# Kernel optimization log

Hardware: AMD Instinct MI355X
Metric: run time of the kernel (lower is better)

Reference implementation:

```python
import jax, jax.numpy as jnp
import numpy as np

N = 100000
E = 1600000
IN_DIM = 128
OUT_DIM = 128
NEG_SLOPE = 0.01  # F.leaky_relu default


def setup_inputs() -> dict:
    key = jax.random.key(0)
    k1, k2, k3, k4, k5, k6 = jax.random.split(key, 6)
    feat = jax.random.normal(k1, (N, IN_DIM), dtype=jnp.float32)
    biclique_mask = jax.random.uniform(k2, (IN_DIM,), dtype=jnp.float32)
    W = jax.random.normal(k3, (OUT_DIM, IN_DIM), dtype=jnp.float32) * 0.05
    attn = jax.random.normal(k4, (OUT_DIM,), dtype=jnp.float32) * 0.1
    src = jax.random.randint(k5, (E,), 0, N, dtype=jnp.int32)
    dst = jax.random.randint(k6, (E,), 0, N, dtype=jnp.int32)
    return {"feat": feat, "biclique_mask": biclique_mask, "W": W,
            "attn": attn, "src": src, "dst": dst}


def reference(feat, biclique_mask, W, attn, src, dst):
    # h = Linear(feat * mask), no bias
    h = (feat * biclique_mask[None, :]) @ W.T            # [N, out_dim]
    # edge score depends only on src node -> compute per-node then gather
    s = jax.nn.leaky_relu(h @ attn, negative_slope=NEG_SLOPE)  # [N]
    score = s[src]                                        # [E]
    # edge softmax grouped by destination node
    seg_max = jax.ops.segment_max(score, dst, num_segments=N)  # [N]
    seg_max = jnp.where(jnp.isfinite(seg_max), seg_max, 0.0)   # empty segs
    ex = jnp.exp(score - seg_max[dst])                     # [E]
    denom = jax.ops.segment_sum(ex, dst, num_segments=N)   # [N]
    a = ex / denom[dst]                                    # [E]
    # weighted aggregation: sum_{e: dst(e)=v} h[src(e)] * a[e]
    m = h[src] * a[:, None]                                # [E, out_dim]
    h_new = jax.ops.segment_sum(m, dst, num_segments=N)    # [N, out_dim]
    return jax.nn.relu(h_new)
```

## Files before the change

kernel.cpp:

```cpp
#include <hip/hip_runtime.h>
#include <math.h>

#define NN 100000
#define EE 1600000
#define DIM 128

#define BK 256
#define NBK2 392
#define NCH 256
#define EPB 6250
#define SCN (NBK2 * NCH)
#define NSB 98

#define GEMM_BLKS 782
#define FBLK 512

#define LDS_ROW 272
#define LDS_B_OFF 34816
#define LDS_TOT 69632

#define SRC_MASK 0x1FFFFu

typedef _Float16 half8 __attribute__((ext_vector_type(8)));
typedef _Float16 half4v __attribute__((ext_vector_type(4)));
typedef signed char char8 __attribute__((ext_vector_type(8)));
typedef float f32x4 __attribute__((ext_vector_type(4)));

__global__ __launch_bounds__(256) void k_wt(const float* __restrict__ W,
                                            const float* __restrict__ mask,
                                            _Float16* __restrict__ Bt) {
    int o = blockIdx.x * 256 + threadIdx.x;
    if (o < DIM * DIM) Bt[o] = (_Float16)(W[o] * mask[o & 127]);
}

__global__ __launch_bounds__(512, 4) void k_front(const float* __restrict__ feat,
                                                  const _Float16* __restrict__ Bt,
                                                  const float* __restrict__ attn,
                                                  signed char* __restrict__ hq,
                                                  float* __restrict__ scf,
                                                  _Float16* __restrict__ sv16,
                                                  const int* __restrict__ dst,
                                                  int* __restrict__ gHist) {
    __shared__ char smem[LDS_TOT];
    const int bx = blockIdx.x;
    const int t  = threadIdx.x;

    if (bx >= GEMM_BLKS) {
        int* hist = (int*)smem;
        const int b = bx - GEMM_BLKS;
        for (int i = t; i < NBK2; i += FBLK) hist[i] = 0;
        __syncthreads();
        const int e0 = b * EPB;
        int e1 = e0 + EPB; if (e1 > EE) e1 = EE;
        for (int e = e0 + t; e < e1; e += FBLK)
            atomicAdd(&hist[dst[e] >> 8], 1);
        __syncthreads();
        for (int i = t; i < NBK2; i += FBLK)
            gHist[i * NCH + b] = hist[i];
        return;
    }

    const int rowBase = bx * 128;

#pragma unroll
    for (int i = 0; i < 8; ++i) {
        int idx  = i * FBLK + t;
        int r    = idx >> 5;
        int c4   = idx & 31;
        int rowg = rowBase + r;
        float4 f = (rowg < NN)
                       ? ((const float4*)(feat + (size_t)rowg * DIM))[c4]
                       : make_float4(0.f, 0.f, 0.f, 0.f);
        half4v h;
        h[0] = (_Float16)f.x; h[1] = (_Float16)f.y;
        h[2] = (_Float16)f.z; h[3] = (_Float16)f.w;
        *(half4v*)(smem + r * LDS_ROW + c4 * 8) = h;
    }
#pragma unroll
    for (int i = 0; i < 4; ++i) {
        int idx = i * FBLK + t;
        int r   = idx >> 4;
        int c8  = idx & 15;
        int4 v = ((const int4*)(Bt + (size_t)r * DIM))[c8];
        *(int4*)(smem + LDS_B_OFF + r * LDS_ROW + c8 * 16) = v;
    }
    __syncthreads();

    const int lane = t & 63;
    const int wv   = t >> 6;
    const int l15  = lane & 15;
    const int quad = lane >> 4;
    const int row0 = rowBase + wv * 16;

    f32x4 acc[8];
#pragma unroll
    for (int nt = 0; nt < 8; ++nt) acc[nt] = (f32x4){0.f, 0.f, 0.f, 0.f};

    const char* Abase = smem + (wv * 16 + l15) * LDS_ROW + quad * 16;
    const char* Bbase = smem + LDS_B_OFF + l15 * LDS_ROW + quad * 16;

#pragma unroll
    for (int kc = 0; kc < 4; ++kc) {
        half8 a = *(const half8*)(Abase + kc * 64);
#pragma unroll
        for (int nt = 0; nt < 8; ++nt) {
            half8 b = *(const half8*)(Bbase + nt * 16 * LDS_ROW + kc * 64);
            acc[nt] = __builtin_amdgcn_mfma_f32_16x16x32_f16(a, b, acc[nt], 0, 0, 0);
        }
    }

    float avv[8];
#pragma unroll
    for (int nt = 0; nt < 8; ++nt) avv[nt] = attn[nt * 16 + l15];

    char* qslice = smem + wv * (16 * LDS_ROW);
#pragma unroll
    for (int r = 0; r < 4; ++r) {
        int row = row0 + quad * 4 + r;
        float p = 0.f, m = 0.f;
#pragma unroll
        for (int nt = 0; nt < 8; ++nt) {
            p += acc[nt][r] * avv[nt];
            m = fmaxf(m, fabsf(acc[nt][r]));
        }
        p += __shfl_xor(p, 1, 64);
        p += __shfl_xor(p, 2, 64);
        p += __shfl_xor(p, 4, 64);
        p += __shfl_xor(p, 8, 64);
        m = fmaxf(m, __shfl_xor(m, 1, 64));
        m = fmaxf(m, __shfl_xor(m, 2, 64));
        m = fmaxf(m, __shfl_xor(m, 4, 64));
        m = fmaxf(m, __shfl_xor(m, 8, 64));
        if (l15 == 0 && row < NN) {
            float lr = (p > 0.f) ? p : 0.01f * p;
            sv16[row] = (_Float16)__expf(lr);
            scf[row]  = m * (1.f / 127.f);
        }
        const float inv_s = (m > 0.f) ? (127.f / m) : 0.f;
#pragma unroll
        for (int nt = 0; nt < 8; ++nt) {
            float qv = rintf(acc[nt][r] * inv_s);
            qv = fminf(fmaxf(qv, -127.f), 127.f);
            qslice[(quad * 4 + r) * 128 + nt * 16 + l15] = (signed char)(int)qv;
        }
    }
    {
        const int rowg = row0 + (lane >> 2);
        if (rowg < NN) {
            int4 v0 = *(const int4*)(qslice + lane * 32);
            int4 v1 = *(const int4*)(qslice + lane * 32 + 16);
            int4* dp = (int4*)(hq + (size_t)rowg * DIM + (lane & 3) * 32);
            dp[0] = v0;
            dp[1] = v1;
        }
    }
}

__global__ __launch_bounds__(256) void k_scan_a(const int* __restrict__ deg,
                                                int* __restrict__ excl,
                                                int* __restrict__ bsum) {
    __shared__ int wsum[4];
    __shared__ int woff[4];
    const int t = threadIdx.x, b = blockIdx.x;
    const int base = b * 1024 + t * 4;
    int v0 = deg[base + 0];
    int v1 = deg[base + 1];
    int v2 = deg[base + 2];
    int v3 = deg[base + 3];
    int tsum = v0 + v1 + v2 + v3;

    const int lane = t & 63, w = t >> 6;
    int incl = tsum;
#pragma unroll
    for (int d = 1; d < 64; d <<= 1) {
        int n = __shfl_up(incl, d, 64);
        if (lane >= d) incl += n;
    }
    if (lane == 63) wsum[w] = incl;
    __syncthreads();
    if (t == 0) {
        int run = 0;
#pragma unroll
        for (int i = 0; i < 4; ++i) { woff[i] = run; run += wsum[i]; }
        bsum[b] = run;
    }
    __syncthreads();
    int texcl = incl - tsum + woff[w];
    excl[base + 0] = texcl;
    excl[base + 1] = texcl + v0;
    excl[base + 2] = texcl + v0 + v1;
    excl[base + 3] = texcl + v0 + v1 + v2;
}

#define INLINE_BOFF_SCAN(bsum, sboff, swtop, t)                          \
    {                                                                    \
        const int lane_ = (t) & 63;                                      \
        int v_ = 0, incl_ = 0;                                           \
        if ((t) < 128) {                                                 \
            v_ = ((t) < NSB) ? (bsum)[(t)] : 0;                          \
            incl_ = v_;                                                  \
            _Pragma("unroll")                                            \
            for (int d_ = 1; d_ < 64; d_ <<= 1) {                        \
                int n_ = __shfl_up(incl_, d_, 64);                       \
                if (lane_ >= d_) incl_ += n_;                            \
            }                                                            \
            if ((t) == 63) (swtop) = incl_;                              \
        }                                                                \
        __syncthreads();                                                 \
        if ((t) < NSB) {                                                 \
            int add_ = ((t) >= 64) ? (swtop) : 0;                        \
            (sboff)[(t)] = incl_ - v_ + add_;                            \
        }                                                                \
        __syncthreads();                                                 \
    }

__global__ __launch_bounds__(1024) void k_bscatter(const int* __restrict__ src,
                                                   const int* __restrict__ dst,
                                                   const int* __restrict__ gOff,
                                                   const int* __restrict__ bsum,
                                                   unsigned* __restrict__ binned) {
    __shared__ int cur[NBK2];
    __shared__ int sboff[NSB];
    __shared__ int swtop;
    const int t = threadIdx.x, b = blockIdx.x;

    INLINE_BOFF_SCAN(bsum, sboff, swtop, t)

    for (int i = t; i < NBK2; i += 1024) {
        int idx = i * NCH + b;
        cur[i] = gOff[idx] + sboff[idx >> 10];
    }
    __syncthreads();
    const int e0 = b * EPB;
    int e1 = e0 + EPB; if (e1 > EE) e1 = EE;
    for (int e = e0 + t; e < e1; e += 1024) {
        int d  = dst[e];
        int si = src[e];
        int bk   = d >> 8;
        int dloc = d & (BK - 1);
        int pos = atomicAdd(&cur[bk], 1);
        binned[pos] = (unsigned)si | ((unsigned)dloc << 17);
    }
}

__global__ __launch_bounds__(1024) void k_group(const int* __restrict__ gOff,
                                                const int* __restrict__ bsum,
                                                const unsigned* __restrict__ binned,
                                                const _Float16* __restrict__ sv16,
                                                const float* __restrict__ scf,
                                                unsigned* __restrict__ pack,
                                                int* __restrict__ offs,
                                                float* __restrict__ lsum) {
    __shared__ int ldeg[BK];
    __shared__ float lsumSh[BK];
    __shared__ int wpart[4];
    __shared__ int sboff[NSB];
    __shared__ int swtop;
    const int bk = blockIdx.x;
    const int t  = threadIdx.x;

    INLINE_BOFF_SCAN(bsum, sboff, swtop, t)

    const int i0 = bk * NCH;
    const int base = gOff[i0] + sboff[i0 >> 10];
    int endp;
    if (bk == NBK2 - 1) endp = EE;
    else {
        int i1 = (bk + 1) * NCH;
        endp = gOff[i1] + sboff[i1 >> 10];
    }

    if (t < BK) { ldeg[t] = 0; lsumSh[t] = 0.f; }
    __syncthreads();
    for (int j = base + t; j < endp; j += 1024)
        atomicAdd(&ldeg[(binned[j] >> 17) & (BK - 1)], 1);
    __syncthreads();

    int v = 0, incl = 0;
    const int lane = t & 63;
    if (t < BK) {
        v = ldeg[t];
        incl = v;
#pragma unroll
        for (int d = 1; d < 64; d <<= 1) {
            int n = __shfl_up(incl, d, 64);
            if (lane >= d) incl += n;
        }
        if (lane == 63) wpart[t >> 6] = incl;
    }
    __syncthreads();
    if (t == 0) {
        int run = 0;
#pragma unroll
        for (int i = 0; i < 4; ++i) { int tmp = wpart[i]; wpart[i] = run; run += tmp; }
    }
    __syncthreads();
    if (t < BK) {
        int excl = incl - v + wpart[t >> 6];
        int c = base + excl;
        int n = bk * BK + t;
        if (n < NN) offs[n] = c;
        ldeg[t] = c;
    }
    if (bk == NBK2 - 1 && t == 0) offs[NN] = EE;
    __syncthreads();

    for (int j = base + t; j < endp; j += 1024) {
        unsigned e = binned[j];
        int dloc = (e >> 17) & (BK - 1);
        int si   = e & SRC_MASK;
        float w  = (float)sv16[si];
        float sc = scf[si];
        unsigned short wb =
            __builtin_bit_cast(unsigned short, (_Float16)(w * sc));
        atomicAdd(&lsumSh[dloc], w);
        int pos = atomicAdd(&ldeg[dloc], 1);
        pack[pos] = (unsigned)si | ((unsigned)wb << 17);
    }
    __syncthreads();
    if (t < BK) {
        int n = bk * BK + t;
        if (n < NN) lsum[n] = lsumSh[t];
    }
}

__global__ __launch_bounds__(256) void k_agg(const signed char* __restrict__ hq,
                                             const int* __restrict__ offs,
                                             const unsigned* __restrict__ pack,
                                             const float* __restrict__ lsum,
                                             float* __restrict__ out) {
    const int lane = threadIdx.x & 63;
    const int g    = lane >> 4;
    const int li   = lane & 15;
    const int wid  = __builtin_amdgcn_readfirstlane(blockIdx.x * 4 + (threadIdx.x >> 6));
    if (wid >= NN) return;
    const int beg = __builtin_amdgcn_readfirstlane(offs[wid]);
    const int end = __builtin_amdgcn_readfirstlane(offs[wid + 1]);

    const signed char* hb = hq + li * 8;
    float acc[8];
#pragma unroll
    for (int k = 0; k < 8; ++k) acc[k] = 0.f;

    int p = beg;
    for (; p + 16 <= end; p += 16) {
        unsigned eb[4];
#pragma unroll
        for (int s = 0; s < 4; ++s) eb[s] = pack[p + s * 4 + g];
        char8 q[4];
#pragma unroll
        for (int s = 0; s < 4; ++s)
            q[s] = *(const char8*)(hb + ((size_t)(eb[s] & SRC_MASK) << 7));
        float wg[4];
#pragma unroll
        for (int s = 0; s < 4; ++s)
            wg[s] = (float)__builtin_bit_cast(_Float16,
                                              (unsigned short)(eb[s] >> 17));
#pragma unroll
        for (int s = 0; s < 4; ++s)
#pragma unroll
            for (int k = 0; k < 8; ++k)
                acc[k] = fmaf((float)q[s][k], wg[s], acc[k]);
    }
    if (p < end) {
        const int last = end - 1;
        unsigned eb[4];
        bool ok[4];
#pragma unroll
        for (int s = 0; s < 4; ++s) {
            int idx = p + s * 4 + g;
            ok[s] = idx < end;
            eb[s] = pack[ok[s] ? idx : last];
        }
        char8 q[4];
#pragma unroll
        for (int s = 0; s < 4; ++s)
            q[s] = *(const char8*)(hb + ((size_t)(eb[s] & SRC_MASK) << 7));
        float wg[4];
#pragma unroll
        for (int s = 0; s < 4; ++s)
            wg[s] = ok[s] ? (float)__builtin_bit_cast(
                                _Float16, (unsigned short)(eb[s] >> 17))
                          : 0.f;
#pragma unroll
        for (int s = 0; s < 4; ++s)
#pragma unroll
            for (int k = 0; k < 8; ++k)
                acc[k] = fmaf((float)q[s][k], wg[s], acc[k]);
    }

#pragma unroll
    for (int k = 0; k < 8; ++k) {
        acc[k] += __shfl_xor(acc[k], 16, 64);
        acc[k] += __shfl_xor(acc[k], 32, 64);
    }

    const float l   = lsum[wid];
    const float inv = (l > 0.f) ? (1.0f / l) : 0.f;

    if (g == 0) {
        float4 o0, o1;
        o0.x = fmaxf(acc[0] * inv, 0.f);
        o0.y = fmaxf(acc[1] * inv, 0.f);
        o0.z = fmaxf(acc[2] * inv, 0.f);
        o0.w = fmaxf(acc[3] * inv, 0.f);
        o1.x = fmaxf(acc[4] * inv, 0.f);
        o1.y = fmaxf(acc[5] * inv, 0.f);
        o1.z = fmaxf(acc[6] * inv, 0.f);
        o1.w = fmaxf(acc[7] * inv, 0.f);
        float4* op = (float4*)(out + (size_t)wid * DIM + li * 8);
        op[0] = o0;
        op[1] = o1;
    }
}

extern "C" void kernel_launch(void* const* d_in, const int* in_sizes, int n_in,
                              void* d_out, int out_size, void* d_ws, size_t ws_size,
                              hipStream_t stream) {
    const float* feat = (const float*)d_in[0];
    const float* mask = (const float*)d_in[1];
    const float* W    = (const float*)d_in[2];
    const float* attn = (const float*)d_in[3];
    const int*   src  = (const int*)d_in[4];
    const int*   dst  = (const int*)d_in[5];
    float* out = (float*)d_out;

    char* ws = (char*)d_ws;
    size_t off = 0;
    auto alloc = [&](size_t bytes) -> void* {
        void* p = ws + off;
        off = (off + bytes + 511) & ~(size_t)511;
        return p;
    };
    signed char* hq  = (signed char*)alloc((size_t)NN * DIM);
    float*   scf  = (float*)alloc((size_t)NN * 4);
    float*   lsum = (float*)alloc((size_t)NN * 4);
    _Float16* sv16 = (_Float16*)alloc((size_t)NN * 2);
    _Float16* Bt   = (_Float16*)alloc((size_t)DIM * DIM * 2);
    int*     gOff  = (int*)alloc((size_t)SCN * 4);
    int*     offs  = (int*)alloc((size_t)(NN + 1) * 4);
    int*     bsum  = (int*)alloc((size_t)NSB * 4);
    unsigned* binned = (unsigned*)alloc((size_t)EE * 4);
    unsigned* pack   = (unsigned*)alloc((size_t)EE * 4);

    k_wt<<<(DIM * DIM + 255) / 256, 256, 0, stream>>>(W, mask, Bt);
    k_front<<<GEMM_BLKS + NCH, FBLK, 0, stream>>>(feat, Bt, attn, hq, scf,
                                                  sv16, dst, gOff);
    k_scan_a<<<NSB, 256, 0, stream>>>(gOff, gOff, bsum);
    k_bscatter<<<NCH, 1024, 0, stream>>>(src, dst, gOff, bsum, binned);
    k_group<<<NBK2, 1024, 0, stream>>>(gOff, bsum, binned, sv16, scf,
                                       pack, offs, lsum);
    k_agg<<<(NN + 3) / 4, 256, 0, stream>>>(hq, offs, pack, lsum, out);
}
```

Measured before the change: 205.4 us.

## Make front kernel persistent with per-block histogram and trim aggregation tail

The fused GEMM+histogram kernel becomes persistent: 512 blocks loop over the 782 row tiles, load Bt and attn once per block, and each block then builds a histogram over half a chunk of edges. Two blocks share a chunk column and add into it atomically, so the histogram buffer is zeroed with a memset first. The aggregation tail also gathers only as many edge groups as remain instead of all four. The aim is to cut block launch and B reloads and wasted tail gathers, at the cost of an extra memset, global atomics, and uneven tile counts per block.

```diff
diff --git a/kernel.cpp b/kernel.cpp
--- a/kernel.cpp
+++ b/kernel.cpp
@@ -8,12 +8,12 @@
 #define BK 256
 #define NBK2 392
 #define NCH 256
-#define EPB 6250
 #define SCN (NBK2 * NCH)
 #define NSB 98
 
-#define GEMM_BLKS 782
-#define FBLK 512
+#define N_TILES 782
+#define FT_BLOCKS 512
+#define HEPB 3125
 
 #define LDS_ROW 272
 #define LDS_B_OFF 34816
@@ -44,116 +44,115 @@
     __shared__ char smem[LDS_TOT];
     const int bx = blockIdx.x;
     const int t  = threadIdx.x;
-
-    if (bx >= GEMM_BLKS) {
-        int* hist = (int*)smem;
-        const int b = bx - GEMM_BLKS;
-        for (int i = t; i < NBK2; i += FBLK) hist[i] = 0;
-        __syncthreads();
-        const int e0 = b * EPB;
-        int e1 = e0 + EPB; if (e1 > EE) e1 = EE;
-        for (int e = e0 + t; e < e1; e += FBLK)
-            atomicAdd(&hist[dst[e] >> 8], 1);
-        __syncthreads();
-        for (int i = t; i < NBK2; i += FBLK)
-            gHist[i * NCH + b] = hist[i];
-        return;
-    }
-
-    const int rowBase = bx * 128;
-
-#pragma unroll
-    for (int i = 0; i < 8; ++i) {
-        int idx  = i * FBLK + t;
-        int r    = idx >> 5;
-        int c4   = idx & 31;
-        int rowg = rowBase + r;
-        float4 f = (rowg < NN)
-                       ? ((const float4*)(feat + (size_t)rowg * DIM))[c4]
-                       : make_float4(0.f, 0.f, 0.f, 0.f);
-        half4v h;
-        h[0] = (_Float16)f.x; h[1] = (_Float16)f.y;
-        h[2] = (_Float16)f.z; h[3] = (_Float16)f.w;
-        *(half4v*)(smem + r * LDS_ROW + c4 * 8) = h;
-    }
+    const int lane = t & 63;
+    const int wv   = t >> 6;
+    const int l15  = lane & 15;
+    const int quad = lane >> 4;
+
 #pragma unroll
     for (int i = 0; i < 4; ++i) {
-        int idx = i * FBLK + t;
+        int idx = i * FT_BLOCKS + t;
         int r   = idx >> 4;
         int c8  = idx & 15;
         int4 v = ((const int4*)(Bt + (size_t)r * DIM))[c8];
         *(int4*)(smem + LDS_B_OFF + r * LDS_ROW + c8 * 16) = v;
     }
-    __syncthreads();
-
-    const int lane = t & 63;
-    const int wv   = t >> 6;
-    const int l15  = lane & 15;
-    const int quad = lane >> 4;
-    const int row0 = rowBase + wv * 16;
-
-    f32x4 acc[8];
-#pragma unroll
-    for (int nt = 0; nt < 8; ++nt) acc[nt] = (f32x4){0.f, 0.f, 0.f, 0.f};
-
-    const char* Abase = smem + (wv * 16 + l15) * LDS_ROW + quad * 16;
-    const char* Bbase = smem + LDS_B_OFF + l15 * LDS_ROW + quad * 16;
-
-#pragma unroll
-    for (int kc = 0; kc < 4; ++kc) {
-        half8 a = *(const half8*)(Abase + kc * 64);
-#pragma unroll
-        for (int nt = 0; nt < 8; ++nt) {
-            half8 b = *(const half8*)(Bbase + nt * 16 * LDS_ROW + kc * 64);
-            acc[nt] = __builtin_amdgcn_mfma_f32_16x16x32_f16(a, b, acc[nt], 0, 0, 0);
+
+    float avv[8];
+#pragma unroll
+    for (int nt = 0; nt < 8; ++nt) avv[nt] = attn[nt * 16 + l15];
+
+    for (int tile = bx; tile < N_TILES; tile += FT_BLOCKS) {
+        const int rowBase = tile * 128;
+
+#pragma unroll
+        for (int i = 0; i < 8; ++i) {
+            int idx  = i * FT_BLOCKS + t;
+            int r    = idx >> 5;
+            int c4   = idx & 31;
+            int rowg = rowBase + r;
+            float4 f = (rowg < NN)
+                           ? ((const float4*)(feat + (size_t)rowg * DIM))[c4]
+                           : make_float4(0.f, 0.f, 0.f, 0.f);
+            half4v h;
+            h[0] = (_Float16)f.x; h[1] = (_Float16)f.y;
+            h[2] = (_Float16)f.z; h[3] = (_Float16)f.w;
+            *(half4v*)(smem + r * LDS_ROW + c4 * 8) = h;
         }
-    }
-
-    float avv[8];
-#pragma unroll
-    for (int nt = 0; nt < 8; ++nt) avv[nt] = attn[nt * 16 + l15];
-
-    char* qslice = smem + wv * (16 * LDS_ROW);
-#pragma unroll
-    for (int r = 0; r < 4; ++r) {
-        int row = row0 + quad * 4 + r;
-        float p = 0.f, m = 0.f;
-#pragma unroll
-        for (int nt = 0; nt < 8; ++nt) {
-            p += acc[nt][r] * avv[nt];
-            m = fmaxf(m, fabsf(acc[nt][r]));
+        __syncthreads();
+
+        const int row0 = rowBase + wv * 16;
+        f32x4 acc[8];
+#pragma unroll
+        for (int nt = 0; nt < 8; ++nt) acc[nt] = (f32x4){0.f, 0.f, 0.f, 0.f};
+
+        const char* Abase = smem + (wv * 16 + l15) * LDS_ROW + quad * 16;
+        const char* Bbase = smem + LDS_B_OFF + l15 * LDS_ROW + quad * 16;
+
+#pragma unroll
+        for (int kc = 0; kc < 4; ++kc) {
+            half8 a = *(const half8*)(Abase + kc * 64);
+#pragma unroll
+            for (int nt = 0; nt < 8; ++nt) {
+                half8 b = *(const half8*)(Bbase + nt * 16 * LDS_ROW + kc * 64);
+                acc[nt] = __builtin_amdgcn_mfma_f32_16x16x32_f16(a, b, acc[nt], 0, 0, 0);
+            }
         }
-        p += __shfl_xor(p, 1, 64);
-        p += __shfl_xor(p, 2, 64);
-        p += __shfl_xor(p, 4, 64);
-        p += __shfl_xor(p, 8, 64);
-        m = fmaxf(m, __shfl_xor(m, 1, 64));
-        m = fmaxf(m, __shfl_xor(m, 2, 64));
-        m = fmaxf(m, __shfl_xor(m, 4, 64));
-        m = fmaxf(m, __shfl_xor(m, 8, 64));
-        if (l15 == 0 && row < NN) {
-            float lr = (p > 0.f) ? p : 0.01f * p;
-            sv16[row] = (_Float16)__expf(lr);
-            scf[row]  = m * (1.f / 127.f);
+
+        char* qslice = smem + wv * (16 * LDS_ROW);
+#pragma unroll
+        for (int r = 0; r < 4; ++r) {
+            int row = row0 + quad * 4 + r;
+            float p = 0.f, m = 0.f;
+#pragma unroll
+            for (int nt = 0; nt < 8; ++nt) {
+                p += acc[nt][r] * avv[nt];
+                m = fmaxf(m, fabsf(acc[nt][r]));
+            }
+            p += __shfl_xor(p, 1, 64);
+            p += __shfl_xor(p, 2, 64);
+            p += __shfl_xor(p, 4, 64);
+            p += __shfl_xor(p, 8, 64);
+            m = fmaxf(m, __shfl_xor(m, 1, 64));
+            m = fmaxf(m, __shfl_xor(m, 2, 64));
+            m = fmaxf(m, __shfl_xor(m, 4, 64));
+            m = fmaxf(m, __shfl_xor(m, 8, 64));
+            if (l15 == 0 && row < NN) {
+                float lr = (p > 0.f) ? p : 0.01f * p;
+                sv16[row] = (_Float16)__expf(lr);
+                scf[row]  = m * (1.f / 127.f);
+            }
+            const float inv_s = (m > 0.f) ? (127.f / m) : 0.f;
+#pragma unroll
+            for (int nt = 0; nt < 8; ++nt) {
+                float qv = rintf(acc[nt][r] * inv_s);
+                qv = fminf(fmaxf(qv, -127.f), 127.f);
+                qslice[(quad * 4 + r) * 128 + nt * 16 + l15] = (signed char)(int)qv;
+            }
         }
-        const float inv_s = (m > 0.f) ? (127.f / m) : 0.f;
-#pragma unroll
-        for (int nt = 0; nt < 8; ++nt) {
-            float qv = rintf(acc[nt][r] * inv_s);
-            qv = fminf(fmaxf(qv, -127.f), 127.f);
-            qslice[(quad * 4 + r) * 128 + nt * 16 + l15] = (signed char)(int)qv;
+        {
+            const int rowg = row0 + (lane >> 2);
+            if (rowg < NN) {
+                int4 v0 = *(const int4*)(qslice + lane * 32);
+                int4 v1 = *(const int4*)(qslice + lane * 32 + 16);
+                int4* dp = (int4*)(hq + (size_t)rowg * DIM + (lane & 3) * 32);
+                dp[0] = v0;
+                dp[1] = v1;
+            }
         }
-    }
-    {
-        const int rowg = row0 + (lane >> 2);
-        if (rowg < NN) {
-            int4 v0 = *(const int4*)(qslice + lane * 32);
-            int4 v1 = *(const int4*)(qslice + lane * 32 + 16);
-            int4* dp = (int4*)(hq + (size_t)rowg * DIM + (lane & 3) * 32);
-            dp[0] = v0;
-            dp[1] = v1;
-        }
-    }
+        __syncthreads();
+    }
+
+    int* hist = (int*)smem;
+    for (int i = t; i < NBK2; i += FT_BLOCKS) hist[i] = 0;
+    __syncthreads();
+    const int e0 = bx * HEPB;
+    for (int e = e0 + t; e < e0 + HEPB; e += FT_BLOCKS)
+        atomicAdd(&hist[dst[e] >> 8], 1);
+    __syncthreads();
+    const int col = bx >> 1;
+    for (int i = t; i < NBK2; i += FT_BLOCKS)
+        atomicAdd(&gHist[i * NCH + col], hist[i]);
 }
 
 __global__ __launch_bounds__(256) void k_scan_a(const int* __restrict__ deg,
@@ -214,6 +213,7 @@
         __syncthreads();                                                 \
     }
 
+#define EPB 6250
 __global__ __launch_bounds__(1024) void k_bscatter(const int* __restrict__ src,
                                                    const int* __restrict__ dst,
                                                    const int* __restrict__ gOff,
@@ -324,6 +324,20 @@
     }
 }
 
+#define TAIL_STEP(S)                                                        \
+    {                                                                       \
+        int idx_ = p + (S) * 4 + g;                                         \
+        bool ok_ = idx_ < end;                                              \
+        unsigned eb_ = pack[ok_ ? idx_ : last];                             \
+        char8 q_ = *(const char8*)(hb + ((size_t)(eb_ & SRC_MASK) << 7));   \
+        float wg_ = ok_ ? (float)__builtin_bit_cast(                        \
+                              _Float16, (unsigned short)(eb_ >> 17))        \
+                        : 0.f;                                              \
+        _Pragma("unroll")                                                   \
+        for (int k_ = 0; k_ < 8; ++k_)                                      \
+            acc[k_] = fmaf((float)q_[k_], wg_, acc[k_]);                    \
+    }
+
 __global__ __launch_bounds__(256) void k_agg(const signed char* __restrict__ hq,
                                              const int* __restrict__ offs,
                                              const unsigned* __restrict__ pack,
@@ -362,31 +376,13 @@
             for (int k = 0; k < 8; ++k)
                 acc[k] = fmaf((float)q[s][k], wg[s], acc[k]);
     }
-    if (p < end) {
+    const int rem = end - p;
+    if (rem > 0) {
         const int last = end - 1;
-        unsigned eb[4];
-        bool ok[4];
-#pragma unroll
-        for (int s = 0; s < 4; ++s) {
-            int idx = p + s * 4 + g;
-            ok[s] = idx < end;
-            eb[s] = pack[ok[s] ? idx : last];
-        }
-        char8 q[4];
-#pragma unroll
-        for (int s = 0; s < 4; ++s)
-            q[s] = *(const char8*)(hb + ((size_t)(eb[s] & SRC_MASK) << 7));
-        float wg[4];
-#pragma unroll
-        for (int s = 0; s < 4; ++s)
-            wg[s] = ok[s] ? (float)__builtin_bit_cast(
-                                _Float16, (unsigned short)(eb[s] >> 17))
-                          : 0.f;
-#pragma unroll
-        for (int s = 0; s < 4; ++s)
-#pragma unroll
-            for (int k = 0; k < 8; ++k)
-                acc[k] = fmaf((float)q[s][k], wg[s], acc[k]);
+        if (rem > 12)      { TAIL_STEP(0) TAIL_STEP(1) TAIL_STEP(2) TAIL_STEP(3) }
+        else if (rem > 8)  { TAIL_STEP(0) TAIL_STEP(1) TAIL_STEP(2) }
+        else if (rem > 4)  { TAIL_STEP(0) TAIL_STEP(1) }
+        else               { TAIL_STEP(0) }
     }
 
 #pragma unroll
@@ -443,9 +439,10 @@
     unsigned* binned = (unsigned*)alloc((size_t)EE * 4);
     unsigned* pack   = (unsigned*)alloc((size_t)EE * 4);
 
+    hipMemsetAsync(gOff, 0, (size_t)SCN * 4, stream);
     k_wt<<<(DIM * DIM + 255) / 256, 256, 0, stream>>>(W, mask, Bt);
-    k_front<<<GEMM_BLKS + NCH, FBLK, 0, stream>>>(feat, Bt, attn, hq, scf,
-                                                  sv16, dst, gOff);
+    k_front<<<FT_BLOCKS, 512, 0, stream>>>(feat, Bt, attn, hq, scf,
+                                           sv16, dst, gOff);
     k_scan_a<<<NSB, 256, 0, stream>>>(gOff, gOff, bsum);
     k_bscatter<<<NCH, 1024, 0, stream>>>(src, dst, gOff, bsum, binned);
     k_group<<<NBK2, 1024, 0, stream>>>(gOff, bsum, binned, sv16, scf,
```

Result: slower. 211.6 us (+3.1%).
